# Performance work log

Measured on AMD Instinct MI355X. Metric: run time of the kernel, lower is better.

Reference implementation:

```python
import jax, jax.numpy as jnp
import numpy as np

B, D, N, P, MAXG, K = 1024, 128, 131072, 64, 2048, 16


def _l2norm(x, eps=1e-12):
    # matches torch F.normalize: x / clamp_min(||x||, eps)
    return x / jnp.maximum(jnp.linalg.norm(x, axis=-1, keepdims=True), eps)


def setup_inputs() -> dict:
    key = jax.random.key(0)
    ks = jax.random.split(key, 7)
    query = jax.random.normal(ks[0], (B, D), jnp.float32)
    keys = jax.random.normal(ks[1], (N, D), jnp.float32)
    vals = jax.random.normal(ks[2], (N, D), jnp.float32)
    labels = jax.random.normal(ks[3], (N,), jnp.float32)
    hard_assignment = jax.random.randint(ks[4], (B,), 0, P)
    cached_groups = jax.random.randint(ks[5], (P, MAXG), 0, N)
    group_sizes = jax.random.randint(ks[6], (P,), K, MAXG + 1)
    # -1 padding beyond each group's size, as in cache_sample_groups
    pos = jnp.arange(MAXG)[None, :]
    cached_groups = jnp.where(pos < group_sizes[:, None], cached_groups, -1)
    return dict(query=query, keys=keys, vals=vals, labels=labels,
                hard_assignment=hard_assignment, cached_groups=cached_groups,
                group_sizes=group_sizes, k=K)


def reference(query, keys, vals, labels, hard_assignment, cached_groups, group_sizes, k):
    n = keys.shape[0]
    q_norm = _l2norm(query)                                  # (B, D)
    grp = group_sizes[hard_assignment]                       # (B,)
    normal = grp >= k                                        # fallback mask (grp<k -> zeros)
    cand = cached_groups[hard_assignment]                    # (B, G) padded with -1
    valid = cand >= 0
    safe = jnp.clip(cand, 0, n - 1)
    keys_c = _l2norm(keys[safe])                             # (B, G, D) gathered + normalized
    sim = jnp.einsum('bd,bgd->bg', q_norm, keys_c)           # cosine similarity
    sim = jnp.where(valid, sim, -1e9)                        # mask padded candidates
    _, top = jax.lax.top_k(sim, k)                           # (B, k) positions within group
    i_final = jnp.take_along_axis(safe, top, axis=1)         # (B, k) memory-bank indices
    nk = keys[i_final]                                       # (B, k, D)
    nv = vals[i_final]                                       # (B, k, D)
    nl = labels[jnp.clip(i_final, 0, n - 1)]                 # (B, k)
    m = normal[:, None]
    nk = jnp.where(m[..., None], nk, 0.0)
    nv = jnp.where(m[..., None], nv, 0.0)
    nl = jnp.where(m, nl, 0.0)
    top_k_idx = jnp.where(m, i_final, 0)
    return nk, nv, nl, top_k_idx
```

## Files before the change

kernel.cpp:

```cpp
#include <hip/hip_runtime.h>

#define DIMS 128
#define KTOP 16
#define SMAX 2048
#define SLICE 64
#define CK 64
#define CQ 16
#define QT 16
#define NTHR 128

__device__ __forceinline__ unsigned long long packsim(float v, int g) {
    unsigned u = __float_as_uint(v);
    u = (u & 0x80000000u) ? ~u : (u | 0x80000000u);
    return ((unsigned long long)u << 32) | (unsigned)(0xFFFFFFFFu - (unsigned)g);
}

__global__ __launch_bounds__(1024)
void bucket_kernel(const int* __restrict__ hard_assign,
                   int* __restrict__ qcount, int* __restrict__ qlist, int B, int P)
{
    const int t = threadIdx.x;
    for (int i = t; i < P; i += 1024) qcount[i] = 0;
    __syncthreads();
    for (int b = t; b < B; b += 1024) {
        const int p = hard_assign[b];
        const int slot = atomicAdd(&qcount[p], 1);
        qlist[(size_t)p * B + slot] = b;
    }
}

__global__ __launch_bounds__(NTHR)
void score_kernel(const float* __restrict__ query,
                  const float* __restrict__ keys,
                  const int*   __restrict__ cached_groups,
                  const int*   __restrict__ qcount,
                  const int*   __restrict__ qlist,
                  float* __restrict__ sims,
                  int B, int N, int MAXG, int nslice)
{
    __shared__ float s_keyT[DIMS * CK];
    __shared__ float s_qT[DIMS * CQ];
    __shared__ float s_inv[SLICE];
    __shared__ int   s_g[SLICE];
    __shared__ int   s_qb[QT];

    const int p = blockIdx.x / nslice;
    const int s = blockIdx.x % nslice;
    const int cnt = qcount[p];
    if (cnt == 0) return;

    const int t = threadIdx.x;
    const int base = s * SLICE;
    const int* gp = cached_groups + (size_t)p * MAXG;
    const int* ql = qlist + (size_t)p * B;

    {
        const int r    = t >> 1;
        const int half = t & 1;
        const int cand = (base + r < MAXG) ? gp[base + r] : -1;
        if (half == 0) s_g[r] = cand;
        const int sf = cand < 0 ? 0 : (cand > N - 1 ? N - 1 : cand);
        const float* kr = keys + (size_t)sf * DIMS + half * 64;
        float ks = 0.0f;
        #pragma unroll
        for (int h = 0; h < 2; ++h) {
            float4 v[8];
            #pragma unroll
            for (int i = 0; i < 8; ++i)
                v[i] = *(const float4*)(kr + h * 32 + i * 4);
            #pragma unroll
            for (int i = 0; i < 8; ++i) {
                const int d = half * 64 + h * 32 + i * 4;
                ks += v[i].x * v[i].x + v[i].y * v[i].y
                    + v[i].z * v[i].z + v[i].w * v[i].w;
                s_keyT[(d + 0) * CK + r] = v[i].x;
                s_keyT[(d + 1) * CK + r] = v[i].y;
                s_keyT[(d + 2) * CK + r] = v[i].z;
                s_keyT[(d + 3) * CK + r] = v[i].w;
            }
        }
        ks += __shfl_xor(ks, 1, 64);
        if (half == 0) s_inv[r] = 1.0f / fmaxf(sqrtf(ks), 1e-12f);
    }

    const int q0 = (t >> 4) * 2;
    const int c0 = (t & 15) * 4;

    for (int qbase = 0; qbase < cnt; qbase += QT) {
        {
            const int q    = t & 15;
            const int dblk = t >> 4;
            const int ii = qbase + q;
            const int sq = ql[(ii < cnt) ? ii : (cnt - 1)];
            if (dblk == 0) s_qb[q] = sq;
            const float* qr = query + (size_t)sq * DIMS + dblk * 16;
            #pragma unroll
            for (int i = 0; i < 4; ++i) {
                const float4 v = *(const float4*)(qr + i * 4);
                const int d = dblk * 16 + i * 4;
                s_qT[(d + 0) * CQ + q] = v.x;
                s_qT[(d + 1) * CQ + q] = v.y;
                s_qT[(d + 2) * CQ + q] = v.z;
                s_qT[(d + 3) * CQ + q] = v.w;
            }
        }
        __syncthreads();

        float acc[2][4];
        #pragma unroll
        for (int a = 0; a < 2; ++a)
            #pragma unroll
            for (int bb = 0; bb < 4; ++bb) acc[a][bb] = 0.0f;

        #pragma unroll 8
        for (int k = 0; k < DIMS; ++k) {
            const float2 aq = *(const float2*)&s_qT[k * CQ + q0];
            const float4 bk = *(const float4*)&s_keyT[k * CK + c0];
            acc[0][0] += aq.x * bk.x; acc[0][1] += aq.x * bk.y;
            acc[0][2] += aq.x * bk.z; acc[0][3] += aq.x * bk.w;
            acc[1][0] += aq.y * bk.x; acc[1][1] += aq.y * bk.y;
            acc[1][2] += aq.y * bk.z; acc[1][3] += aq.y * bk.w;
        }

        const float4 inv = *(const float4*)&s_inv[c0];
        const int4   gv  = *(const int4*)&s_g[c0];
        #pragma unroll
        for (int qi = 0; qi < 2; ++qi) {
            const int ii = qbase + q0 + qi;
            if (ii < cnt) {
                const int b = s_qb[q0 + qi];
                float4 o;
                o.x = (gv.x >= 0) ? acc[qi][0] * inv.x : -1.0e9f;
                o.y = (gv.y >= 0) ? acc[qi][1] * inv.y : -1.0e9f;
                o.z = (gv.z >= 0) ? acc[qi][2] * inv.z : -1.0e9f;
                o.w = (gv.w >= 0) ? acc[qi][3] * inv.w : -1.0e9f;
                float* dst = sims + (size_t)b * MAXG + base + c0;
                if (base + c0 + 3 < MAXG) {
                    *(float4*)dst = o;
                } else {
                    if (base + c0 + 0 < MAXG) dst[0] = o.x;
                    if (base + c0 + 1 < MAXG) dst[1] = o.y;
                    if (base + c0 + 2 < MAXG) dst[2] = o.z;
                }
            }
        }

        if (qbase + QT < cnt) __syncthreads();
    }
}

__global__ __launch_bounds__(256)
void topk_gather_kernel(const float* __restrict__ keys,
                        const float* __restrict__ vals,
                        const float* __restrict__ labels,
                        const int*   __restrict__ hard_assign,
                        const int*   __restrict__ cached_groups,
                        const int*   __restrict__ group_sizes,
                        const float* __restrict__ sims,
                        float* __restrict__ out,
                        int B, int MAXG)
{
    const int b = blockIdx.x, t = threadIdx.x;
    const int lane = t & 63, w = t >> 6;
    const int sub = t & 15, cg = t >> 4;

    __shared__ unsigned long long s_merge[64];
    __shared__ int s_wing[KTOP];

    const int p = hard_assign[b];
    const int grpsz = group_sizes[p];
    const bool normal = (grpsz >= KTOP);
    const int* gptr = cached_groups + (size_t)p * MAXG;
    const float* simrow = sims + (size_t)b * MAXG;

    unsigned long long mk[SMAX / 256];
    #pragma unroll
    for (int j = 0; j < SMAX / 256; ++j) {
        const int g = w * (SMAX / 4) + j * 64 + lane;
        const float v = (g < MAXG) ? simrow[g] : -3.0e38f;
        mk[j] = packsim(v, g);
    }
    #pragma unroll 1
    for (int r = 0; r < KTOP; ++r) {
        unsigned long long m = mk[0];
        #pragma unroll
        for (int j = 1; j < SMAX / 256; ++j) m = (mk[j] > m) ? mk[j] : m;
        #pragma unroll
        for (int off = 1; off < 64; off <<= 1) {
            unsigned long long o = __shfl_xor(m, off, 64);
            m = (o > m) ? o : m;
        }
        if (lane == 0) s_merge[w * KTOP + r] = m;
        #pragma unroll
        for (int j = 0; j < SMAX / 256; ++j) if (mk[j] == m) mk[j] = 0ull;
    }
    __syncthreads();

    if (w == 0) {
        unsigned long long u = s_merge[lane];
        #pragma unroll 1
        for (int r = 0; r < KTOP; ++r) {
            unsigned long long m = u;
            #pragma unroll
            for (int off = 1; off < 64; off <<= 1) {
                unsigned long long o = __shfl_xor(m, off, 64);
                m = (o > m) ? o : m;
            }
            if (lane == 0)
                s_wing[r] = (int)(0xFFFFFFFFu - (unsigned)(m & 0xFFFFFFFFull));
            if (u == m) u = 0ull;
        }
    }
    __syncthreads();

    const int g    = s_wing[cg];
    const int cand = gptr[g];
    const int idx  = cand < 0 ? 0 : cand;

    const size_t BK = (size_t)B * KTOP;
    float* out_nk = out;
    float* out_nv = out + BK * DIMS;
    float* out_nl = out + 2 * BK * DIMS;
    float* out_id = out_nl + BK;

    const size_t od = ((size_t)b * KTOP + cg) * DIMS + sub * 8;
    if (normal) {
        const float* kr = keys + (size_t)idx * DIMS + sub * 8;
        const float* vr = vals + (size_t)idx * DIMS + sub * 8;
        *(float4*)(out_nk + od)     = *(const float4*)(kr);
        *(float4*)(out_nk + od + 4) = *(const float4*)(kr + 4);
        *(float4*)(out_nv + od)     = *(const float4*)(vr);
        *(float4*)(out_nv + od + 4) = *(const float4*)(vr + 4);
        if (sub == 0) {
            out_nl[(size_t)b * KTOP + cg] = labels[idx];
            out_id[(size_t)b * KTOP + cg] = (float)idx;
        }
    } else {
        const float4 z = make_float4(0.f, 0.f, 0.f, 0.f);
        *(float4*)(out_nk + od)     = z;
        *(float4*)(out_nk + od + 4) = z;
        *(float4*)(out_nv + od)     = z;
        *(float4*)(out_nv + od + 4) = z;
        if (sub == 0) {
            out_nl[(size_t)b * KTOP + cg] = 0.0f;
            out_id[(size_t)b * KTOP + cg] = 0.0f;
        }
    }
}

extern "C" void kernel_launch(void* const* d_in, const int* in_sizes, int n_in,
                              void* d_out, int out_size, void* d_ws, size_t ws_size,
                              hipStream_t stream) {
    const float* query  = (const float*)d_in[0];
    const float* keys   = (const float*)d_in[1];
    const float* vals   = (const float*)d_in[2];
    const float* labels = (const float*)d_in[3];
    const int* hard_assign   = (const int*)d_in[4];
    const int* cached_groups = (const int*)d_in[5];
    const int* group_sizes   = (const int*)d_in[6];

    const int B = in_sizes[0] / DIMS;
    const int N = in_sizes[1] / DIMS;
    const int P = in_sizes[6];
    const int MAXG = in_sizes[5] / P;
    const int nslice = (MAXG + SLICE - 1) / SLICE;

    float* sims  = (float*)d_ws;
    int* qcount  = (int*)((char*)d_ws + (size_t)B * MAXG * 4);
    int* qlist   = qcount + P;

    bucket_kernel<<<1, 1024, 0, stream>>>(hard_assign, qcount, qlist, B, P);

    score_kernel<<<P * nslice, NTHR, 0, stream>>>(
        query, keys, cached_groups, qcount, qlist, sims, B, N, MAXG, nslice);

    topk_gather_kernel<<<B, 256, 0, stream>>>(
        keys, vals, labels, hard_assign, cached_groups, group_sizes, sims,
        (float*)d_out, B, MAXG);
}
```

Before: 60.16 us.

## Fuse query bucketing into score kernel and presort per-lane top-k candidates

Drops the separate single-block bucket kernel. Each score block now builds its partition's query list in shared memory with a wavefront ballot/popcount scan over hard_assign, which removes one launch and a serialized dependency at the cost of every block rescanning all B assignments. In the top-k kernel, each lane sorts its 8 packed candidates once with a sorting network. Each selection round then only reads the head element and shifts on a match, instead of doing an 8-way max and a compare-clear pass. Query lists are capped at QLMAX, so a partition with more matching queries than that would silently drop them.

```diff
diff --git a/kernel.cpp b/kernel.cpp
--- a/kernel.cpp
+++ b/kernel.cpp
@@ -8,6 +8,7 @@
 #define CQ 16
 #define QT 16
 #define NTHR 128
+#define QLMAX 2048
 
 __device__ __forceinline__ unsigned long long packsim(float v, int g) {
     unsigned u = __float_as_uint(v);
@@ -15,26 +16,11 @@
     return ((unsigned long long)u << 32) | (unsigned)(0xFFFFFFFFu - (unsigned)g);
 }
 
-__global__ __launch_bounds__(1024)
-void bucket_kernel(const int* __restrict__ hard_assign,
-                   int* __restrict__ qcount, int* __restrict__ qlist, int B, int P)
-{
-    const int t = threadIdx.x;
-    for (int i = t; i < P; i += 1024) qcount[i] = 0;
-    __syncthreads();
-    for (int b = t; b < B; b += 1024) {
-        const int p = hard_assign[b];
-        const int slot = atomicAdd(&qcount[p], 1);
-        qlist[(size_t)p * B + slot] = b;
-    }
-}
-
 __global__ __launch_bounds__(NTHR)
 void score_kernel(const float* __restrict__ query,
                   const float* __restrict__ keys,
                   const int*   __restrict__ cached_groups,
-                  const int*   __restrict__ qcount,
-                  const int*   __restrict__ qlist,
+                  const int*   __restrict__ hard_assign,
                   float* __restrict__ sims,
                   int B, int N, int MAXG, int nslice)
 {
@@ -43,16 +29,33 @@
     __shared__ float s_inv[SLICE];
     __shared__ int   s_g[SLICE];
     __shared__ int   s_qb[QT];
+    __shared__ int   s_ql[QLMAX];
+    __shared__ int   s_cnt;
 
     const int p = blockIdx.x / nslice;
     const int s = blockIdx.x % nslice;
-    const int cnt = qcount[p];
+    const int t = threadIdx.x;
+
+    if (t < 64) {
+        int running = 0;
+        for (int r0 = 0; r0 < B; r0 += 64) {
+            const int b = r0 + t;
+            const bool match = (b < B) && (hard_assign[b] == p);
+            const unsigned long long mask = __ballot(match);
+            if (match) {
+                const int pre = __popcll(mask & ((1ull << t) - 1ull));
+                if (running + pre < QLMAX) s_ql[running + pre] = b;
+            }
+            running += __popcll(mask);
+        }
+        if (t == 0) s_cnt = (running < QLMAX) ? running : QLMAX;
+    }
+    __syncthreads();
+    const int cnt = s_cnt;
     if (cnt == 0) return;
 
-    const int t = threadIdx.x;
     const int base = s * SLICE;
     const int* gp = cached_groups + (size_t)p * MAXG;
-    const int* ql = qlist + (size_t)p * B;
 
     {
         const int r    = t >> 1;
@@ -91,7 +94,7 @@
             const int q    = t & 15;
             const int dblk = t >> 4;
             const int ii = qbase + q;
-            const int sq = ql[(ii < cnt) ? ii : (cnt - 1)];
+            const int sq = s_ql[(ii < cnt) ? ii : (cnt - 1)];
             if (dblk == 0) s_qb[q] = sq;
             const float* qr = query + (size_t)sq * DIMS + dblk * 16;
             #pragma unroll
@@ -149,6 +152,8 @@
     }
 }
 
+#define CASW(x,y) { if ((x) < (y)) { const unsigned long long _t = (x); (x) = (y); (y) = _t; } }
+
 __global__ __launch_bounds__(256)
 void topk_gather_kernel(const float* __restrict__ keys,
                         const float* __restrict__ vals,
@@ -173,26 +178,35 @@
     const int* gptr = cached_groups + (size_t)p * MAXG;
     const float* simrow = sims + (size_t)b * MAXG;
 
-    unsigned long long mk[SMAX / 256];
-    #pragma unroll
-    for (int j = 0; j < SMAX / 256; ++j) {
-        const int g = w * (SMAX / 4) + j * 64 + lane;
-        const float v = (g < MAXG) ? simrow[g] : -3.0e38f;
-        mk[j] = packsim(v, g);
-    }
+    unsigned long long k0, k1, k2, k3, k4, k5, k6, k7;
+    {
+        #define LDK(j) ({ const int g = w * (SMAX / 4) + (j) * 64 + lane;          \
+                          const float v = (g < MAXG) ? simrow[g] : -3.0e38f;       \
+                          packsim(v, g); })
+        k0 = LDK(0); k1 = LDK(1); k2 = LDK(2); k3 = LDK(3);
+        k4 = LDK(4); k5 = LDK(5); k6 = LDK(6); k7 = LDK(7);
+        #undef LDK
+    }
+    CASW(k0,k1) CASW(k2,k3) CASW(k4,k5) CASW(k6,k7)
+    CASW(k0,k2) CASW(k1,k3) CASW(k4,k6) CASW(k5,k7)
+    CASW(k1,k2) CASW(k5,k6)
+    CASW(k0,k4) CASW(k1,k5) CASW(k2,k6) CASW(k3,k7)
+    CASW(k2,k4) CASW(k3,k5)
+    CASW(k1,k2) CASW(k3,k4) CASW(k5,k6)
+
     #pragma unroll 1
     for (int r = 0; r < KTOP; ++r) {
-        unsigned long long m = mk[0];
-        #pragma unroll
-        for (int j = 1; j < SMAX / 256; ++j) m = (mk[j] > m) ? mk[j] : m;
+        unsigned long long wm = k0;
         #pragma unroll
         for (int off = 1; off < 64; off <<= 1) {
-            unsigned long long o = __shfl_xor(m, off, 64);
-            m = (o > m) ? o : m;
-        }
-        if (lane == 0) s_merge[w * KTOP + r] = m;
-        #pragma unroll
-        for (int j = 0; j < SMAX / 256; ++j) if (mk[j] == m) mk[j] = 0ull;
+            const unsigned long long o = __shfl_xor(wm, off, 64);
+            wm = (o > wm) ? o : wm;
+        }
+        if (lane == 0) s_merge[w * KTOP + r] = wm;
+        if (k0 == wm) {
+            k0 = k1; k1 = k2; k2 = k3; k3 = k4;
+            k4 = k5; k5 = k6; k6 = k7; k7 = 0ull;
+        }
     }
     __syncthreads();
 
@@ -203,7 +217,7 @@
             unsigned long long m = u;
             #pragma unroll
             for (int off = 1; off < 64; off <<= 1) {
-                unsigned long long o = __shfl_xor(m, off, 64);
+                const unsigned long long o = __shfl_xor(m, off, 64);
                 m = (o > m) ? o : m;
             }
             if (lane == 0)
@@ -265,14 +279,10 @@
     const int MAXG = in_sizes[5] / P;
     const int nslice = (MAXG + SLICE - 1) / SLICE;
 
-    float* sims  = (float*)d_ws;
-    int* qcount  = (int*)((char*)d_ws + (size_t)B * MAXG * 4);
-    int* qlist   = qcount + P;
-
-    bucket_kernel<<<1, 1024, 0, stream>>>(hard_assign, qcount, qlist, B, P);
+    float* sims = (float*)d_ws;
 
     score_kernel<<<P * nslice, NTHR, 0, stream>>>(
-        query, keys, cached_groups, qcount, qlist, sims, B, N, MAXG, nslice);
+        query, keys, cached_groups, hard_assign, sims, B, N, MAXG, nslice);
 
     topk_gather_kernel<<<B, 256, 0, stream>>>(
         keys, vals, labels, hard_assign, cached_groups, group_sizes, sims,
```

Result: slower. 66.29 us (+10.2%).
